# Kernel tuning notes

Measured on AMD Instinct MI355X. Metric: run time of the kernel, lower is better.

## Reference

```python
import jax, jax.numpy as jnp
import numpy as np

N_TOKEN = 267735
CUTS = [0, 20000, 40000, 200000, 267735]
DIV = 4
D_MODEL = 1024
N_HEAD = 16
D_HEAD = 64
D_INNER = 4096
N_LAYER = 4
QLEN = 512
MLEN = 512
BSZ = 4
EPS = 1e-5


def _ln(x, g, b):
    mu = jnp.mean(x, axis=-1, keepdims=True)
    var = jnp.var(x, axis=-1, keepdims=True)
    return (x - mu) * jax.lax.rsqrt(var + EPS) * g + b


def _rel_shift(x):
    # x: [qlen, klen, bsz, n_head]
    q, k, b, n = x.shape
    x = jnp.pad(x, ((0, 0), (1, 0), (0, 0), (0, 0)))
    x = x.reshape(k + 1, q, b, n)[1:]
    return x.reshape(q, k, b, n)


def setup_inputs() -> dict:
    key = jax.random.key(0)
    ks = list(jax.random.split(key, 32))
    p = lambda i, shape: 0.02 * jax.random.normal(ks[i], shape, dtype=jnp.float32)
    inp = {}
    inp['input_ids'] = jax.random.randint(ks[0], (BSZ, QLEN), 0, N_TOKEN, dtype=jnp.int32)
    inp['mems'] = 0.05 * jax.random.normal(ks[1], (N_LAYER, MLEN, BSZ, D_MODEL), dtype=jnp.float32)
    # adaptive embedding: cluster tables + projections (div_val=4)
    for i in range(4):
        l, r = CUTS[i], CUTS[i + 1]
        d_i = D_MODEL // (DIV ** i)
        inp[f'emb{i}'] = p(2 + i, (r - l, d_i))
        inp[f'proj{i}'] = p(6 + i, (d_i, D_MODEL))
    H = N_HEAD * D_HEAD
    inp['qkv_W'] = p(10, (N_LAYER, D_MODEL, 3 * H))
    inp['r_W'] = p(11, (N_LAYER, D_MODEL, H))
    inp['o_W'] = p(12, (N_LAYER, H, D_MODEL))
    inp['r_w_bias'] = p(13, (N_LAYER, N_HEAD, D_HEAD))
    inp['r_r_bias'] = p(14, (N_LAYER, N_HEAD, D_HEAD))
    inp['ln1_g'] = jnp.ones((N_LAYER, D_MODEL), jnp.float32)
    inp['ln1_b'] = jnp.zeros((N_LAYER, D_MODEL), jnp.float32)
    inp['ff_w1'] = p(15, (N_LAYER, D_MODEL, D_INNER))
    inp['ff_b1'] = jnp.zeros((N_LAYER, D_INNER), jnp.float32)
    inp['ff_w2'] = p(16, (N_LAYER, D_INNER, D_MODEL))
    inp['ff_b2'] = jnp.zeros((N_LAYER, D_MODEL), jnp.float32)
    inp['ln2_g'] = jnp.ones((N_LAYER, D_MODEL), jnp.float32)
    inp['ln2_b'] = jnp.zeros((N_LAYER, D_MODEL), jnp.float32)
    return inp


def _forward(input_ids, mems, embs, projs, qkv_W, r_W, o_W, r_w_bias, r_r_bias,
             ln1_g, ln1_b, ff_w1, ff_b1, ff_w2, ff_b2, ln2_g, ln2_b):
    ids = input_ids.T  # [qlen, bsz]
    qlen, bsz = ids.shape
    mems = jax.lax.stop_gradient(mems)  # mems are detached in the original
    mlen = mems.shape[1]
    klen = qlen + mlen

    # --- adaptive embedding (masked gather + scatter-add, same math as boolean_mask/scatter_nd) ---
    flat = ids.reshape(-1)
    emb = jnp.zeros((flat.shape[0], D_MODEL), jnp.float32)
    for i in range(4):
        l, r = CUTS[i], CUTS[i + 1]
        mask = (flat >= l) & (flat < r)
        idx = jnp.clip(flat - l, 0, r - l - 1)
        e_i = jnp.einsum('id,de->ie', embs[i][idx], projs[i])
        emb = emb + jnp.where(mask[:, None], e_i, 0.0)
    word_emb = (emb * (D_MODEL ** 0.5)).reshape(qlen, bsz, D_MODEL)

    # --- sinusoidal relative positions, pos_seq = klen-1 .. 0 ---
    pos_seq = jnp.arange(klen - 1, -1, -1, dtype=jnp.float32)
    inv_freq = 1.0 / (10000.0 ** (jnp.arange(0, D_MODEL, 2, dtype=jnp.float32) / D_MODEL))
    sinusoid = jnp.einsum('i,j->ij', pos_seq, inv_freq)
    pos_emb = jnp.concatenate([jnp.sin(sinusoid), jnp.cos(sinusoid)], axis=-1)  # [klen, d_model]

    # causal mask over memory-extended keys: [qlen, klen]
    attn_mask = jnp.triu(jnp.ones((qlen, klen), jnp.float32), k=1 + mlen)
    mask4 = attn_mask[:, :, None, None]
    scale = 1.0 / (D_HEAD ** 0.5)

    h = word_emb
    for l in range(N_LAYER):
        cat = jnp.concatenate([mems[l], h], axis=0)  # [klen, bsz, d_model]
        w_heads = jnp.einsum('kbd,dh->kbh', cat, qkv_W[l])
        r_head_k = jnp.einsum('kd,dh->kh', pos_emb, r_W[l]).reshape(klen, N_HEAD, D_HEAD)
        q_h, k_h, v_h = jnp.split(w_heads, 3, axis=-1)
        q_h = q_h[-qlen:].reshape(qlen, bsz, N_HEAD, D_HEAD)
        k_h = k_h.reshape(klen, bsz, N_HEAD, D_HEAD)
        v_h = v_h.reshape(klen, bsz, N_HEAD, D_HEAD)
        AC = jnp.einsum('ibnd,jbnd->ijbn', q_h + r_w_bias[l], k_h)
        BD = _rel_shift(jnp.einsum('ibnd,jnd->ijbn', q_h + r_r_bias[l], r_head_k))
        score = (AC + BD) * scale
        score = score * (1.0 - mask4) - 1e30 * mask4
        prob = jax.nn.softmax(score, axis=1)
        attn_vec = jnp.einsum('ijbn,jbnd->ibnd', prob, v_h).reshape(qlen, bsz, N_HEAD * D_HEAD)
        attn_out = jnp.einsum('ibh,hd->ibd', attn_vec, o_W[l])
        h = _ln(h + attn_out, ln1_g[l], ln1_b[l])
        ff = jnp.einsum('ibf,fd->ibd', jax.nn.relu(jnp.einsum('ibd,df->ibf', h, ff_w1[l]) + ff_b1[l]), ff_w2[l]) + ff_b2[l]
        h = _ln(h + ff, ln2_g[l], ln2_b[l])

    return h.transpose(1, 0, 2)  # [bsz, qlen, d_model]


def reference(input_ids, mems, emb0, emb1, emb2, emb3, proj0, proj1, proj2, proj3,
              qkv_W, r_W, o_W, r_w_bias, r_r_bias, ln1_g, ln1_b,
              ff_w1, ff_b1, ff_w2, ff_b2, ln2_g, ln2_b):
    return _forward(input_ids, mems, (emb0, emb1, emb2, emb3), (proj0, proj1, proj2, proj3),
                    qkv_W, r_W, o_W, r_w_bias, r_r_bias, ln1_g, ln1_b,
                    ff_w1, ff_b1, ff_w2, ff_b2, ln2_g, ln2_b)
```

## Files before the change

### kernel.cpp

```cpp
#include <hip/hip_runtime.h>

typedef __attribute__((ext_vector_type(8))) short bf16x8;
typedef __attribute__((ext_vector_type(4))) float f32x4;

#define N_LAYER 4
#define QLEN 512
#define MLEN 512
#define KLEN 1024
#define BSZ 4
#define DM 1024
#define NH 16
#define DH 64
#define DINNER 4096
#define EK 1408

__device__ __forceinline__ unsigned short f2bf(float x) {
    unsigned u = __float_as_uint(x);
    u += 0x7fffu + ((u >> 16) & 1u);
    return (unsigned short)(u >> 16);
}
__device__ __forceinline__ float bf2f(unsigned short v) {
    return __uint_as_float(((unsigned)v) << 16);
}

__device__ __forceinline__ void gload16(const unsigned short* g, unsigned short* l) {
    __builtin_amdgcn_global_load_lds(
        (const __attribute__((address_space(1))) unsigned int*)g,
        (__attribute__((address_space(3))) unsigned int*)l, 16, 0, 0);
}

__device__ __forceinline__ bf16x8 lds_read8_sw(const unsigned short* base, int row, int cb) {
    return *(const bf16x8*)((const char*)base + row * 128 + (cb ^ ((row & 7) << 4)));
}

__global__ __launch_bounds__(256)
void transpose_all(const float* __restrict__ qkvWl, const float* __restrict__ rWl,
                   const float* __restrict__ oWl, const float* __restrict__ w1l,
                   const float* __restrict__ w2l,
                   unsigned short* __restrict__ qkvT, unsigned short* __restrict__ rT,
                   unsigned short* __restrict__ oT, unsigned short* __restrict__ w1T,
                   unsigned short* __restrict__ w2T) {
    __shared__ float tile[32][33];
    int id = blockIdx.x;
    const float* W; unsigned short* D; int K, N, bx, by;
    if (id < 3072)      { W = qkvWl; D = qkvT; K = 1024; N = 3072; bx = id % 96;  by = id / 96; }
    else if (id < 4096) { id -= 3072; W = rWl;  D = rT;  K = 1024; N = 1024; bx = id & 31; by = id >> 5; }
    else if (id < 5120) { id -= 4096; W = oWl;  D = oT;  K = 1024; N = 1024; bx = id & 31; by = id >> 5; }
    else if (id < 9216) { id -= 5120; W = w1l;  D = w1T; K = 1024; N = 4096; bx = id & 127; by = id >> 7; }
    else                { id -= 9216; W = w2l;  D = w2T; K = 4096; N = 1024; bx = id & 31; by = id >> 5; }
    const int tx = threadIdx.x & 31, ty = threadIdx.x >> 5;
#pragma unroll
    for (int i = 0; i < 4; ++i)
        tile[ty + i * 8][tx] = W[(size_t)(by * 32 + ty + i * 8) * N + bx * 32 + tx];
    __syncthreads();
#pragma unroll
    for (int i = 0; i < 4; ++i)
        D[(size_t)(bx * 32 + ty + i * 8) * K + by * 32 + tx] = f2bf(tile[tx][ty + i * 8]);
}

__global__ __launch_bounds__(256)
void transpose_pad(const float* __restrict__ W, unsigned short* __restrict__ dst,
                   int K, int N, int dstLD, int dstOff) {
    __shared__ float tile[32][33];
    const int tx = threadIdx.x & 31, ty = threadIdx.x >> 5;
    const int bx = blockIdx.x, by = blockIdx.y;
#pragma unroll
    for (int i = 0; i < 4; ++i) {
        int k = by * 32 + ty + i * 8;
        tile[ty + i * 8][tx] = (k < K) ? W[(size_t)k * N + bx * 32 + tx] : 0.f;
    }
    __syncthreads();
#pragma unroll
    for (int i = 0; i < 4; ++i) {
        int n = bx * 32 + ty + i * 8;
        int k = by * 32 + tx;
        dst[(size_t)n * dstLD + dstOff + k] = f2bf(tile[tx][ty + i * 8]);
    }
}

__global__ __launch_bounds__(256)
void emb_gather(const int* __restrict__ ids,
                const float* __restrict__ e0, const float* __restrict__ e1,
                const float* __restrict__ e2, const float* __restrict__ e3,
                unsigned short* __restrict__ embA) {
    const int chunk = blockIdx.x * 256 + threadIdx.x;
    if (chunk >= 2048 * 176) return;
    const int t = chunk / 176;
    const int e8 = (chunk - t * 176) * 8;
    const int i = t >> 2, b = t & 3;
    const int id = ids[b * QLEN + i];
    const float* src = nullptr;
    if (e8 < 1024) {
        if (id < 20000) src = e0 + (size_t)id * 1024 + e8;
    } else if (e8 < 1280) {
        if (id >= 20000 && id < 40000) src = e1 + (size_t)(id - 20000) * 256 + (e8 - 1024);
    } else if (e8 < 1344) {
        if (id >= 40000 && id < 200000) src = e2 + (size_t)(id - 40000) * 64 + (e8 - 1280);
    } else if (e8 < 1360) {
        if (id >= 200000) src = e3 + (size_t)(id - 200000) * 16 + (e8 - 1344);
    }
    uint4 o = {0u, 0u, 0u, 0u};
    if (src) {
        float4 v0 = *(const float4*)src;
        float4 v1 = *(const float4*)(src + 4);
        o.x = (unsigned)f2bf(v0.x * 32.f) | ((unsigned)f2bf(v0.y * 32.f) << 16);
        o.y = (unsigned)f2bf(v0.z * 32.f) | ((unsigned)f2bf(v0.w * 32.f) << 16);
        o.z = (unsigned)f2bf(v1.x * 32.f) | ((unsigned)f2bf(v1.y * 32.f) << 16);
        o.w = (unsigned)f2bf(v1.z * 32.f) | ((unsigned)f2bf(v1.w * 32.f) << 16);
    }
    *(uint4*)(embA + (size_t)t * EK + e8) = o;
}

template <int MODE, int BN>
__global__ __launch_bounds__(256)
void gemm_bt(const unsigned short* __restrict__ A, const unsigned short* __restrict__ BT,
             float* __restrict__ C, unsigned short* __restrict__ Cbf,
             const float* __restrict__ bias,
             const float* __restrict__ rwb, const float* __restrict__ rrb,
             unsigned short* __restrict__ Qw, unsigned short* __restrict__ Qr,
             unsigned short* __restrict__ Kb, unsigned short* __restrict__ VTb,
             int M, int N, int K) {
    constexpr int NF = BN / 32;
    __shared__ unsigned short lA[2][128 * 64];
    __shared__ unsigned short lB[2][BN * 64];
    const int tid = threadIdx.x;
    const int w = tid >> 6, l = tid & 63;
    const int lane15 = l & 15, lh = l >> 4;
    const int bm = blockIdx.y, bn = blockIdx.x;
    const int wr = (w >> 1) * 64, wc = (w & 1) * (BN / 2);

    f32x4 acc[4][NF] = {};

    const unsigned short* gA = A + (size_t)(bm * 128) * K;
    const unsigned short* gB = BT + (size_t)(bn * BN) * K;

    auto stage = [&](int buf, int k0) {
#pragma unroll
        for (int s = 0; s < 4; ++s) {
            int g = tid + s * 256, row = g >> 3;
            gload16(gA + (size_t)row * K + k0 + ((g & 7) ^ (row & 7)) * 8,
                    lA[buf] + g * 8);
        }
#pragma unroll
        for (int s = 0; s < BN / 32; ++s) {
            int g = tid + s * 256, row = g >> 3;
            gload16(gB + (size_t)row * K + k0 + ((g & 7) ^ (row & 7)) * 8,
                    lB[buf] + g * 8);
        }
    };

    stage(0, 0);
    __syncthreads();
    int cur = 0;
    for (int k0 = 0; k0 < K; k0 += 64) {
        if (k0 + 64 < K) stage(cur ^ 1, k0 + 64);
        const unsigned short* cA = lA[cur];
        const unsigned short* cB = lB[cur];
#pragma unroll
        for (int kk = 0; kk < 2; ++kk) {
            bf16x8 af[4], bfr[NF];
#pragma unroll
            for (int f = 0; f < 4; ++f)
                af[f] = lds_read8_sw(cA, wr + f * 16 + lane15, kk * 64 + lh * 16);
#pragma unroll
            for (int f = 0; f < NF; ++f)
                bfr[f] = lds_read8_sw(cB, wc + f * 16 + lane15, kk * 64 + lh * 16);
#pragma unroll
            for (int mi = 0; mi < 4; ++mi)
#pragma unroll
                for (int ni = 0; ni < NF; ++ni)
                    acc[mi][ni] = __builtin_amdgcn_mfma_f32_16x16x32_bf16(
                        af[mi], bfr[ni], acc[mi][ni], 0, 0, 0);
        }
        __syncthreads();
        cur ^= 1;
    }

#pragma unroll
    for (int mi = 0; mi < 4; ++mi) {
        int rowb = bm * 128 + wr + mi * 16 + lh * 4;
#pragma unroll
        for (int ni = 0; ni < NF; ++ni) {
            int col = bn * BN + wc + ni * 16 + lane15;
#pragma unroll
            for (int r = 0; r < 4; ++r) {
                float x = acc[mi][ni][r];
                if (MODE == 0) {
                    C[(size_t)(rowb + r) * N + col] = x;
                } else if (MODE == 1) {
                    x += bias[col];
                    Cbf[(size_t)(rowb + r) * N + col] = f2bf(x > 0.f ? x : 0.f);
                } else if (MODE == 2) {
                    C[(size_t)(rowb + r) * N + col] = x + bias[col];
                } else if (MODE == 3) {
                    int j = rowb >> 2;
                    int bb_ = r;
                    if (col < 1024) {
                        if (j >= MLEN) {
                            int i = j - MLEN, n = col >> 6, d = col & 63;
                            size_t o = ((size_t)(bb_ * NH + n) * QLEN + i) * DH + d;
                            Qw[o] = f2bf(x + rwb[col]);
                            Qr[o] = f2bf(x + rrb[col]);
                        }
                    } else if (col < 2048) {
                        int c2 = col - 1024, n = c2 >> 6, d = c2 & 63;
                        Kb[((size_t)(bb_ * NH + n) * KLEN + j) * DH + d] = f2bf(x);
                    } else {
                        int c2 = col - 2048, n = c2 >> 6, d = c2 & 63;
                        VTb[((size_t)(bb_ * NH + n) * DH + d) * KLEN + j] = f2bf(x);
                    }
                } else {
                    int j = rowb + r;
                    int n = col >> 6, d = col & 63;
                    Kb[((size_t)n * KLEN + j) * DH + d] = f2bf(x);
                }
            }
        }
    }
}

__global__ __launch_bounds__(256)
void pos_kernel(unsigned short* __restrict__ posbf) {
    const int p = blockIdx.x, tid = threadIdx.x;
    const float ps = (float)(KLEN - 1 - p);
    const float c = -2.0f * 9.210340371976184f / 1024.0f;
#pragma unroll
    for (int j4 = 0; j4 < 4; ++j4) {
        int j = tid + j4 * 256;
        int m = (j < 512) ? j : j - 512;
        float freq = __expf((float)m * c);
        float ang = ps * freq;
        float v = (j < 512) ? sinf(ang) : cosf(ang);
        posbf[(size_t)p * DM + j] = f2bf(v);
    }
}

__global__ __launch_bounds__(256)
void cat_kernel(const float* __restrict__ mem_l, const float* __restrict__ h,
                unsigned short* __restrict__ catbf) {
    const int t = blockIdx.x, tid = threadIdx.x;
    const float* src = (t < 2048) ? (mem_l + (size_t)t * DM) : (h + (size_t)(t - 2048) * DM);
    float4 v = ((const float4*)src)[tid];
    uint2 o;
    o.x = (unsigned)f2bf(v.x) | ((unsigned)f2bf(v.y) << 16);
    o.y = (unsigned)f2bf(v.z) | ((unsigned)f2bf(v.w) << 16);
    ((uint2*)(catbf + (size_t)t * DM))[tid] = o;
}

__global__ __launch_bounds__(512)
void attn_kernel(const unsigned short* __restrict__ Qw, const unsigned short* __restrict__ Qr,
                 const unsigned short* __restrict__ Kb, const unsigned short* __restrict__ VTb,
                 const unsigned short* __restrict__ Rb, unsigned short* __restrict__ avec) {
    __shared__ float lBD[8][16 * 83];
    __shared__ unsigned short lP[8][16 * 64];

    const int tid = threadIdx.x;
    const int w = tid >> 6, l = tid & 63;
    const int wp = w & 3, jg = w >> 2;
    const int lane15 = l & 15, lh = l >> 4;
    const int blk = blockIdx.x;
    const int bn = blk & 63;
    const int it = blk >> 6;
    const int n = bn & 15, b = bn >> 4;
    const int i0 = it * 64;
    const int rowl = wp * 16 + lh * 4;

    bf16x8 qw[2], qr[2];
    {
        size_t qb = ((size_t)bn * QLEN + i0 + wp * 16 + lane15) * DH + lh * 8;
        qw[0] = *(const bf16x8*)(Qw + qb);
        qw[1] = *(const bf16x8*)(Qw + qb + 32);
        qr[0] = *(const bf16x8*)(Qr + qb);
        qr[1] = *(const bf16x8*)(Qr + qb + 32);
    }

    const unsigned short* Kh = Kb + (size_t)bn * KLEN * DH;
    const unsigned short* Vh = VTb + (size_t)bn * DH * KLEN;
    const unsigned short* Rh = Rb + (size_t)n * KLEN * DH;

    f32x4 oacc[4] = {};
    float mrow[4], srow[4];
#pragma unroll
    for (int r = 0; r < 4; ++r) { mrow[r] = -1e30f; srow[r] = 0.f; }

    const int ntiles = it + 9;
    for (int jt = jg; jt < ntiles; jt += 2) {
        const int j0 = jt * 64;
        bf16x8 kf[2][4], rf[2][5];
#pragma unroll
        for (int f = 0; f < 4; ++f) {
            const unsigned short* p = Kh + (size_t)(j0 + f * 16 + lane15) * DH + lh * 8;
            kf[0][f] = *(const bf16x8*)p;
            kf[1][f] = *(const bf16x8*)(p + 32);
        }
#pragma unroll
        for (int f = 0; f < 5; ++f) {
            int rr = 496 + 64 * (jt - it) - 16 * wp + 16 * f + lane15;
            if (rr > 1023) rr = 1023;
            const unsigned short* p = Rh + (size_t)rr * DH + lh * 8;
            rf[0][f] = *(const bf16x8*)p;
            rf[1][f] = *(const bf16x8*)(p + 32);
        }

        f32x4 sac[4] = {};
        f32x4 bd[5] = {};
        __builtin_amdgcn_s_setprio(1);
#pragma unroll
        for (int kk = 0; kk < 2; ++kk) {
#pragma unroll
            for (int f = 0; f < 4; ++f)
                sac[f] = __builtin_amdgcn_mfma_f32_16x16x32_bf16(qw[kk], kf[kk][f], sac[f], 0, 0, 0);
#pragma unroll
            for (int f = 0; f < 5; ++f)
                bd[f] = __builtin_amdgcn_mfma_f32_16x16x32_bf16(qr[kk], rf[kk][f], bd[f], 0, 0, 0);
        }
        __builtin_amdgcn_s_setprio(0);

#pragma unroll
        for (int f = 0; f < 5; ++f)
#pragma unroll
            for (int r = 0; r < 4; ++r)
                lBD[w][(lh * 4 + r) * 83 + lane15 + 16 * f] = bd[f][r];

        float pv[4][4];
        float tmax[4] = {-1e30f, -1e30f, -1e30f, -1e30f};
        const bool lastTile = (jt == it + 8);
#pragma unroll
        for (int f = 0; f < 4; ++f) {
            int lj = lane15 + 16 * f;
#pragma unroll
            for (int r = 0; r < 4; ++r) {
                int cc = 15 + lj - lh * 4 - r;
                float s = (sac[f][r] + lBD[w][(lh * 4 + r) * 83 + cc]) * 0.125f;
                if (lastTile && (lj > rowl + r)) s = -1e30f;
                pv[f][r] = s;
                tmax[r] = fmaxf(tmax[r], s);
            }
        }
#pragma unroll
        for (int off = 1; off < 16; off <<= 1)
#pragma unroll
            for (int r = 0; r < 4; ++r)
                tmax[r] = fmaxf(tmax[r], __shfl_xor(tmax[r], off));

        bool grow = false;
#pragma unroll
        for (int r = 0; r < 4; ++r) grow = grow || (tmax[r] > mrow[r] + 8.f);
        if (__any(grow)) {
#pragma unroll
            for (int r = 0; r < 4; ++r) {
                float nm = fmaxf(mrow[r], tmax[r]);
                float sc = __expf(mrow[r] - nm);
                mrow[r] = nm;
                srow[r] *= sc;
#pragma unroll
                for (int f = 0; f < 4; ++f) oacc[f][r] *= sc;
            }
        }
        float tsum[4];
#pragma unroll
        for (int r = 0; r < 4; ++r) {
            float ts = 0.f;
#pragma unroll
            for (int f = 0; f < 4; ++f) {
                float e = __expf(pv[f][r] - mrow[r]);
                pv[f][r] = e;
                ts += e;
            }
            tsum[r] = ts;
        }
#pragma unroll
        for (int off = 1; off < 16; off <<= 1)
#pragma unroll
            for (int r = 0; r < 4; ++r)
                tsum[r] += __shfl_xor(tsum[r], off);
#pragma unroll
        for (int r = 0; r < 4; ++r) srow[r] += tsum[r];

#pragma unroll
        for (int f = 0; f < 4; ++f)
#pragma unroll
            for (int r = 0; r < 4; ++r) {
                int row = lh * 4 + r, cb2 = (lane15 + 16 * f) * 2;
                *(unsigned short*)((char*)lP[w] + row * 128 + (cb2 ^ ((row & 7) << 4))) =
                    f2bf(pv[f][r]);
            }
        bf16x8 pa[2];
        pa[0] = lds_read8_sw(lP[w], lane15, lh * 16);
        pa[1] = lds_read8_sw(lP[w], lane15, 64 + lh * 16);

        __builtin_amdgcn_s_setprio(1);
#pragma unroll
        for (int kk = 0; kk < 2; ++kk) {
#pragma unroll
            for (int f = 0; f < 4; ++f) {
                bf16x8 vb = *(const bf16x8*)(Vh + (size_t)(f * 16 + lane15) * KLEN + j0 + kk * 32 + lh * 8);
                oacc[f] = __builtin_amdgcn_mfma_f32_16x16x32_bf16(pa[kk], vb, oacc[f], 0, 0, 0);
            }
        }
        __builtin_amdgcn_s_setprio(0);
    }

    __syncthreads();
    float* og = (float*)&lBD[wp][0];
    float* mg = (float*)&lBD[4 + wp][0];
    if (jg == 1) {
#pragma unroll
        for (int f = 0; f < 4; ++f)
#pragma unroll
            for (int r = 0; r < 4; ++r)
                og[(lh * 4 + r) * 65 + lane15 + 16 * f] = oacc[f][r];
        if (lane15 == 0) {
#pragma unroll
            for (int r = 0; r < 4; ++r) {
                mg[lh * 4 + r] = mrow[r];
                mg[16 + lh * 4 + r] = srow[r];
            }
        }
    }
    __syncthreads();
    if (jg == 0) {
#pragma unroll
        for (int r = 0; r < 4; ++r) {
            float m2 = mg[lh * 4 + r], s2 = mg[16 + lh * 4 + r];
            float m = fmaxf(mrow[r], m2);
            float a1 = __expf(mrow[r] - m), a2 = __expf(m2 - m);
            float inv = 1.0f / (srow[r] * a1 + s2 * a2);
            int i = i0 + rowl + r;
            int t = i * 4 + b;
#pragma unroll
            for (int f = 0; f < 4; ++f) {
                float o2 = og[(lh * 4 + r) * 65 + lane15 + 16 * f];
                int col = n * 64 + lane15 + 16 * f;
                avec[(size_t)t * DM + col] = f2bf((oacc[f][r] * a1 + o2 * a2) * inv);
            }
        }
    }
}

__global__ __launch_bounds__(256)
void ln_kernel(const float* __restrict__ hin, const float* __restrict__ res,
               const float* __restrict__ g, const float* __restrict__ bb,
               float* __restrict__ hout, unsigned short* __restrict__ hbf) {
    __shared__ float ls[8];
    const int t = blockIdx.x, tid = threadIdx.x;
    float4 x = ((const float4*)(hin + (size_t)t * DM))[tid];
    float4 rr = ((const float4*)(res + (size_t)t * DM))[tid];
    float v0 = x.x + rr.x, v1 = x.y + rr.y, v2 = x.z + rr.z, v3 = x.w + rr.w;
    float s = v0 + v1 + v2 + v3;
    float sq = v0 * v0 + v1 * v1 + v2 * v2 + v3 * v3;
#pragma unroll
    for (int off = 1; off < 64; off <<= 1) {
        s += __shfl_xor(s, off);
        sq += __shfl_xor(sq, off);
    }
    const int w = tid >> 6;
    if ((tid & 63) == 0) { ls[w] = s; ls[4 + w] = sq; }
    __syncthreads();
    s = ls[0] + ls[1] + ls[2] + ls[3];
    sq = ls[4] + ls[5] + ls[6] + ls[7];
    float mu = s * (1.f / 1024.f);
    float var = sq * (1.f / 1024.f) - mu * mu;
    float rstd = rsqrtf(var + 1e-5f);
    float y[4] = {v0, v1, v2, v3};
    float4 of;
    uint2 ob;
    float* op = &of.x;
#pragma unroll
    for (int j = 0; j < 4; ++j) {
        int d = tid * 4 + j;
        op[j] = (y[j] - mu) * rstd * g[d] + bb[d];
    }
    ob.x = (unsigned)f2bf(of.x) | ((unsigned)f2bf(of.y) << 16);
    ob.y = (unsigned)f2bf(of.z) | ((unsigned)f2bf(of.w) << 16);
    ((float4*)(hout + (size_t)t * DM))[tid] = of;
    ((uint2*)(hbf + (size_t)t * DM))[tid] = ob;
}

__global__ __launch_bounds__(256)
void out_kernel(const float* __restrict__ h, float* __restrict__ out) {
    const int t = blockIdx.x, tid = threadIdx.x;
    const int i = t >> 2, b = t & 3;
    ((float4*)(out + ((size_t)b * QLEN + i) * DM))[tid] =
        ((const float4*)(h + (size_t)t * DM))[tid];
}

extern "C" void kernel_launch(void* const* d_in, const int* in_sizes, int n_in,
                              void* d_out, int out_size, void* d_ws, size_t ws_size,
                              hipStream_t stream) {
    const int* ids = (const int*)d_in[0];
    const float* mems = (const float*)d_in[1];
    const float* embp[4] = {nullptr, nullptr, nullptr, nullptr};
    const float* projp[4] = {nullptr, nullptr, nullptr, nullptr};
    const long long esz[4] = {20000LL * 1024, 20000LL * 256, 160000LL * 64, 67735LL * 16};
    const long long psz[4] = {1024LL * 1024, 256LL * 1024, 64LL * 1024, 16LL * 1024};
    for (int idx = 2; idx <= 9 && idx < n_in; ++idx) {
        long long s = in_sizes[idx];
        for (int c = 0; c < 4; ++c) {
            if (s == esz[c]) embp[c] = (const float*)d_in[idx];
            else if (s == psz[c]) projp[c] = (const float*)d_in[idx];
        }
    }
    const float* qkvW = (const float*)d_in[10];
    const float* rW   = (const float*)d_in[11];
    const float* oW   = (const float*)d_in[12];
    const float* rwb  = (const float*)d_in[13];
    const float* rrb  = (const float*)d_in[14];
    const float* ln1g = (const float*)d_in[15];
    const float* ln1b = (const float*)d_in[16];
    const float* ffw1 = (const float*)d_in[17];
    const float* ffb1 = (const float*)d_in[18];
    const float* ffw2 = (const float*)d_in[19];
    const float* ffb2 = (const float*)d_in[20];
    const float* ln2g = (const float*)d_in[21];
    const float* ln2b = (const float*)d_in[22];

    size_t off = 0;
    char* base = (char*)d_ws;
    auto alloc = [&](size_t bytes) -> char* {
        char* p = base + off;
        off = (off + bytes + 255) & ~(size_t)255;
        return p;
    };
    unsigned short* qkvT  = (unsigned short*)alloc(3072ull * 1024 * 2);
    unsigned short* rT    = (unsigned short*)alloc(1024ull * 1024 * 2);
    unsigned short* oT    = (unsigned short*)alloc(1024ull * 1024 * 2);
    unsigned short* w1T   = (unsigned short*)alloc(4096ull * 1024 * 2);
    unsigned short* w2T   = (unsigned short*)alloc(1024ull * 4096 * 2);
    unsigned short* embA  = (unsigned short*)alloc(2048ull * EK * 2);
    unsigned short* embBT = (unsigned short*)alloc(1024ull * EK * 2);
    float* h              = (float*)alloc(2048ull * 1024 * 4);
    unsigned short* hbf   = (unsigned short*)alloc(2048ull * 1024 * 2);
    unsigned short* catb  = (unsigned short*)alloc(4096ull * 1024 * 2);
    unsigned short* posb  = (unsigned short*)alloc(1024ull * 1024 * 2);
    unsigned short* Qw    = (unsigned short*)alloc(4ull * 16 * 512 * 64 * 2);
    unsigned short* Qr    = (unsigned short*)alloc(4ull * 16 * 512 * 64 * 2);
    unsigned short* Kb    = (unsigned short*)alloc(4ull * 16 * 1024 * 64 * 2);
    unsigned short* VTb   = (unsigned short*)alloc(4ull * 16 * 1024 * 64 * 2);
    unsigned short* Rb    = (unsigned short*)alloc(16ull * 1024 * 64 * 2);
    unsigned short* avec  = (unsigned short*)alloc(2048ull * 1024 * 2);
    float* resid          = (float*)alloc(2048ull * 1024 * 4);
    unsigned short* ff1b  = (unsigned short*)alloc(2048ull * 4096 * 2);
    (void)ws_size; (void)out_size;

    emb_gather<<<(2048 * 176 + 255) / 256, 256, 0, stream>>>(
        ids, embp[0], embp[1], embp[2], embp[3], embA);
    transpose_pad<<<dim3(32, 32), 256, 0, stream>>>(projp[0], embBT, 1024, 1024, EK, 0);
    transpose_pad<<<dim3(32, 8),  256, 0, stream>>>(projp[1], embBT, 256,  1024, EK, 1024);
    transpose_pad<<<dim3(32, 2),  256, 0, stream>>>(projp[2], embBT, 64,   1024, EK, 1280);
    transpose_pad<<<dim3(32, 2),  256, 0, stream>>>(projp[3], embBT, 16,   1024, EK, 1344);
    pos_kernel<<<1024, 256, 0, stream>>>(posb);
    gemm_bt<0, 128><<<dim3(1024 / 128, 2048 / 128), 256, 0, stream>>>(
        embA, embBT, h, nullptr, nullptr, nullptr, nullptr, nullptr, nullptr, nullptr, nullptr,
        2048, 1024, EK);

    for (int l = 0; l < N_LAYER; ++l) {
        const float* qkvWl = qkvW + (size_t)l * 1024 * 3072;
        const float* rWl   = rW + (size_t)l * 1024 * 1024;
        const float* oWl   = oW + (size_t)l * 1024 * 1024;
        const float* w1l   = ffw1 + (size_t)l * 1024 * 4096;
        const float* w2l   = ffw2 + (size_t)l * 4096 * 1024;

        transpose_all<<<13312, 256, 0, stream>>>(qkvWl, rWl, oWl, w1l, w2l,
                                                 qkvT, rT, oT, w1T, w2T);

        cat_kernel<<<4096, 256, 0, stream>>>(mems + (size_t)l * 2048 * 1024, h, catb);

        gemm_bt<3, 128><<<dim3(3072 / 128, 4096 / 128), 256, 0, stream>>>(
            catb, qkvT, nullptr, nullptr, nullptr,
            rwb + l * 1024, rrb + l * 1024, Qw, Qr, Kb, VTb, 4096, 3072, 1024);

        gemm_bt<4, 64><<<dim3(1024 / 64, 1024 / 128), 256, 0, stream>>>(
            posb, rT, nullptr, nullptr, nullptr,
            nullptr, nullptr, nullptr, nullptr, Rb, nullptr, 1024, 1024, 1024);

        attn_kernel<<<512, 512, 0, stream>>>(Qw, Qr, Kb, VTb, Rb, avec);

        gemm_bt<0, 64><<<dim3(1024 / 64, 2048 / 128), 256, 0, stream>>>(
            avec, oT, resid, nullptr, nullptr, nullptr, nullptr, nullptr, nullptr, nullptr, nullptr,
            2048, 1024, 1024);
        ln_kernel<<<2048, 256, 0, stream>>>(h, resid, ln1g + l * 1024, ln1b + l * 1024, h, hbf);

        gemm_bt<1, 128><<<dim3(4096 / 128, 2048 / 128), 256, 0, stream>>>(
            hbf, w1T, nullptr, ff1b, ffb1 + l * 4096, nullptr, nullptr, nullptr, nullptr, nullptr, nullptr,
            2048, 4096, 1024);
        gemm_bt<2, 64><<<dim3(1024 / 64, 2048 / 128), 256, 0, stream>>>(
            ff1b, w2T, resid, nullptr, ffb2 + l * 1024, nullptr, nullptr, nullptr, nullptr, nullptr, nullptr,
            2048, 1024, 4096);
        ln_kernel<<<2048, 256, 0, stream>>>(h, resid, ln2g + l * 1024, ln2b + l * 1024, h, hbf);
    }

    out_kernel<<<2048, 256, 0, stream>>>(h, (float*)d_out);
}
```

Measured before the change: 1.177 ms.

## Swizzle GEMM blocks across XCDs and split attention into smaller reversed-order blocks

GEMM launches become 1D grids with a block-index swizzle that puts contiguous output tiles on the same XCD, aiming for better L2 reuse on the chiplet GPU. The attention kernel now uses 256-thread blocks covering 32 query rows instead of 64, launched as 1024 blocks with the heaviest causal tiles scheduled first, which should improve occupancy and load balance. V fragments are also loaded earlier so their latency overlaps the softmax. The causal-mask and tile-count arithmetic is rewritten to match, which carries correctness risk at tile boundaries.

```diff
diff --git a/kernel.cpp b/kernel.cpp
--- a/kernel.cpp
+++ b/kernel.cpp
@@ -126,7 +126,11 @@
     const int tid = threadIdx.x;
     const int w = tid >> 6, l = tid & 63;
     const int lane15 = l & 15, lh = l >> 4;
-    const int bm = blockIdx.y, bn = blockIdx.x;
+    const int nwg = gridDim.x;
+    const int cpx = nwg >> 3;
+    const int swz = (blockIdx.x & 7) * cpx + (blockIdx.x >> 3);
+    const int nbn = N / BN;
+    const int bm = swz / nbn, bn = swz % nbn;
     const int wr = (w >> 1) * 64, wc = (w & 1) * (BN / 2);
 
     f32x4 acc[4][NF] = {};
@@ -247,23 +251,23 @@
     ((uint2*)(catbf + (size_t)t * DM))[tid] = o;
 }
 
-__global__ __launch_bounds__(512)
+__global__ __launch_bounds__(256, 4)
 void attn_kernel(const unsigned short* __restrict__ Qw, const unsigned short* __restrict__ Qr,
                  const unsigned short* __restrict__ Kb, const unsigned short* __restrict__ VTb,
                  const unsigned short* __restrict__ Rb, unsigned short* __restrict__ avec) {
-    __shared__ float lBD[8][16 * 83];
-    __shared__ unsigned short lP[8][16 * 64];
+    __shared__ float lBD[4][16 * 83];
+    __shared__ unsigned short lP[4][16 * 64];
 
     const int tid = threadIdx.x;
     const int w = tid >> 6, l = tid & 63;
-    const int wp = w & 3, jg = w >> 2;
+    const int wp = w & 1, jg = w >> 1;
     const int lane15 = l & 15, lh = l >> 4;
     const int blk = blockIdx.x;
     const int bn = blk & 63;
-    const int it = blk >> 6;
+    const int it = 15 - (blk >> 6);
     const int n = bn & 15, b = bn >> 4;
-    const int i0 = it * 64;
-    const int rowl = wp * 16 + lh * 4;
+    const int i0 = it * 32;
+    const int rowi = wp * 16 + lh * 4;
 
     bf16x8 qw[2], qr[2];
     {
@@ -283,7 +287,7 @@
 #pragma unroll
     for (int r = 0; r < 4; ++r) { mrow[r] = -1e30f; srow[r] = 0.f; }
 
-    const int ntiles = it + 9;
+    const int ntiles = (607 + 32 * it) >> 6;
     for (int jt = jg; jt < ntiles; jt += 2) {
         const int j0 = jt * 64;
         bf16x8 kf[2][4], rf[2][5];
@@ -293,9 +297,10 @@
             kf[0][f] = *(const bf16x8*)p;
             kf[1][f] = *(const bf16x8*)(p + 32);
         }
+        const int rbase = 496 + 64 * jt - 32 * it - 16 * wp;
 #pragma unroll
         for (int f = 0; f < 5; ++f) {
-            int rr = 496 + 64 * (jt - it) - 16 * wp + 16 * f + lane15;
+            int rr = rbase + 16 * f + lane15;
             if (rr > 1023) rr = 1023;
             const unsigned short* p = Rh + (size_t)rr * DH + lh * 8;
             rf[0][f] = *(const bf16x8*)p;
@@ -316,6 +321,14 @@
         }
         __builtin_amdgcn_s_setprio(0);
 
+        bf16x8 vf[2][4];
+#pragma unroll
+        for (int kk = 0; kk < 2; ++kk)
+#pragma unroll
+            for (int f = 0; f < 4; ++f)
+                vf[kk][f] = *(const bf16x8*)(Vh + (size_t)(f * 16 + lane15) * KLEN +
+                                             j0 + kk * 32 + lh * 8);
+
 #pragma unroll
         for (int f = 0; f < 5; ++f)
 #pragma unroll
@@ -324,7 +337,7 @@
 
         float pv[4][4];
         float tmax[4] = {-1e30f, -1e30f, -1e30f, -1e30f};
-        const bool lastTile = (jt == it + 8);
+        const bool lastTile = (jt == ntiles - 1);
 #pragma unroll
         for (int f = 0; f < 4; ++f) {
             int lj = lane15 + 16 * f;
@@ -332,7 +345,7 @@
             for (int r = 0; r < 4; ++r) {
                 int cc = 15 + lj - lh * 4 - r;
                 float s = (sac[f][r] + lBD[w][(lh * 4 + r) * 83 + cc]) * 0.125f;
-                if (lastTile && (lj > rowl + r)) s = -1e30f;
+                if (lastTile && (j0 + lj > i0 + rowi + r + 512)) s = -1e30f;
                 pv[f][r] = s;
                 tmax[r] = fmaxf(tmax[r], s);
             }
@@ -391,19 +404,16 @@
 
         __builtin_amdgcn_s_setprio(1);
 #pragma unroll
-        for (int kk = 0; kk < 2; ++kk) {
-#pragma unroll
-            for (int f = 0; f < 4; ++f) {
-                bf16x8 vb = *(const bf16x8*)(Vh + (size_t)(f * 16 + lane15) * KLEN + j0 + kk * 32 + lh * 8);
-                oacc[f] = __builtin_amdgcn_mfma_f32_16x16x32_bf16(pa[kk], vb, oacc[f], 0, 0, 0);
-            }
-        }
+        for (int kk = 0; kk < 2; ++kk)
+#pragma unroll
+            for (int f = 0; f < 4; ++f)
+                oacc[f] = __builtin_amdgcn_mfma_f32_16x16x32_bf16(pa[kk], vf[kk][f], oacc[f], 0, 0, 0);
         __builtin_amdgcn_s_setprio(0);
     }
 
     __syncthreads();
     float* og = (float*)&lBD[wp][0];
-    float* mg = (float*)&lBD[4 + wp][0];
+    float* mg = (float*)&lBD[2 + wp][0];
     if (jg == 1) {
 #pragma unroll
         for (int f = 0; f < 4; ++f)
@@ -426,7 +436,7 @@
             float m = fmaxf(mrow[r], m2);
             float a1 = __expf(mrow[r] - m), a2 = __expf(m2 - m);
             float inv = 1.0f / (srow[r] * a1 + s2 * a2);
-            int i = i0 + rowl + r;
+            int i = i0 + rowi + r;
             int t = i * 4 + b;
 #pragma unroll
             for (int f = 0; f < 4; ++f) {
@@ -550,7 +560,7 @@
     transpose_pad<<<dim3(32, 2),  256, 0, stream>>>(projp[2], embBT, 64,   1024, EK, 1280);
     transpose_pad<<<dim3(32, 2),  256, 0, stream>>>(projp[3], embBT, 16,   1024, EK, 1344);
     pos_kernel<<<1024, 256, 0, stream>>>(posb);
-    gemm_bt<0, 128><<<dim3(1024 / 128, 2048 / 128), 256, 0, stream>>>(
+    gemm_bt<0, 128><<<(2048 / 128) * (1024 / 128), 256, 0, stream>>>(
         embA, embBT, h, nullptr, nullptr, nullptr, nullptr, nullptr, nullptr, nullptr, nullptr,
         2048, 1024, EK);
 
@@ -566,25 +576,25 @@
 
         cat_kernel<<<4096, 256, 0, stream>>>(mems + (size_t)l * 2048 * 1024, h, catb);
 
-        gemm_bt<3, 128><<<dim3(3072 / 128, 4096 / 128), 256, 0, stream>>>(
+        gemm_bt<3, 128><<<(4096 / 128) * (3072 / 128), 256, 0, stream>>>(
             catb, qkvT, nullptr, nullptr, nullptr,
             rwb + l * 1024, rrb + l * 1024, Qw, Qr, Kb, VTb, 4096, 3072, 1024);
 
-        gemm_bt<4, 64><<<dim3(1024 / 64, 1024 / 128), 256, 0, stream>>>(
+        gemm_bt<4, 64><<<(1024 / 128) * (1024 / 64), 256, 0, stream>>>(
             posb, rT, nullptr, nullptr, nullptr,
             nullptr, nullptr, nullptr, nullptr, Rb, nullptr, 1024, 1024, 1024);
 
-        attn_kernel<<<512, 512, 0, stream>>>(Qw, Qr, Kb, VTb, Rb, avec);
-
-        gemm_bt<0, 64><<<dim3(1024 / 64, 2048 / 128), 256, 0, stream>>>(
+        attn_kernel<<<1024, 256, 0, stream>>>(Qw, Qr, Kb, VTb, Rb, avec);
+
+        gemm_bt<0, 64><<<(2048 / 128) * (1024 / 64), 256, 0, stream>>>(
             avec, oT, resid, nullptr, nullptr, nullptr, nullptr, nullptr, nullptr, nullptr, nullptr,
             2048, 1024, 1024);
         ln_kernel<<<2048, 256, 0, stream>>>(h, resid, ln1g + l * 1024, ln1b + l * 1024, h, hbf);
 
-        gemm_bt<1, 128><<<dim3(4096 / 128, 2048 / 128), 256, 0, stream>>>(
+        gemm_bt<1, 128><<<(2048 / 128) * (4096 / 128), 256, 0, stream>>>(
             hbf, w1T, nullptr, ff1b, ffb1 + l * 4096, nullptr, nullptr, nullptr, nullptr, nullptr, nullptr,
             2048, 4096, 1024);
-        gemm_bt<2, 64><<<dim3(1024 / 64, 2048 / 128), 256, 0, stream>>>(
+        gemm_bt<2, 64><<<(2048 / 128) * (1024 / 64), 256, 0, stream>>>(
             ff1b, w2T, resid, nullptr, ffb2 + l * 1024, nullptr, nullptr, nullptr, nullptr, nullptr, nullptr,
             2048, 1024, 4096);
         ln_kernel<<<2048, 256, 0, stream>>>(h, resid, ln2g + l * 1024, ln2b + l * 1024, h, hbf);
```

Measured after the change: 1.303 ms. +10.7%, slower.
